# Optimization experiments

Hardware: AMD Instinct MI355X
Metric: run time of the kernel (lower is better)

Reference implementation:

```python
import jax, jax.numpy as jnp
import numpy as np

NUM_HEADS = 16


def setup_inputs() -> dict:
    key = jax.random.key(0)
    ks = jax.random.split(key, 5)
    N, L, E = 4, 1024, 1024
    x = jax.random.normal(ks[0], (N, L, E), dtype=jnp.float32)
    sc = 1.0 / np.sqrt(E)
    wq = jax.random.normal(ks[1], (E, E), dtype=jnp.float32) * sc
    wk = jax.random.normal(ks[2], (E, E), dtype=jnp.float32) * sc
    wv = jax.random.normal(ks[3], (E, E), dtype=jnp.float32) * sc
    wo = jax.random.normal(ks[4], (E, E), dtype=jnp.float32) * sc
    return {"x": x, "wq": wq, "wk": wk, "wv": wv, "wo": wo}


def reference(x, wq, wk, wv, wo):
    N, L, E = x.shape
    H = NUM_HEADS
    d = E // H  # d_k = d_v = d_q
    # Linear layers: y = x @ W^T (torch Linear weight is (out, in))
    q = (x @ wq.T).reshape(N, H, L, d)  # NOTE: raw view, matches torch .view
    k = (x @ wk.T).reshape(N, H, L, d)
    v = (x @ wv.T).reshape(N, H, L, d)
    scores = jnp.einsum("nhld,nhmd->nhlm", q, k) / jnp.sqrt(jnp.float32(d))
    # causal mask (dropout is identity in eval / p=0)
    causal = jnp.tril(jnp.ones((L, L), dtype=bool))
    scores = jnp.where(causal, scores, jnp.float32(-jnp.inf))
    attn = jax.nn.softmax(scores, axis=-1)
    wei = jnp.einsum("nhlm,nhmd->nhld", attn, v).reshape(N, L, H * d)
    return wei @ wo.T
```

## Files before the change

### kernel.cpp

```cpp
#include <hip/hip_runtime.h>
#include <hip/hip_bf16.h>

using bf16 = __hip_bfloat16;
typedef __attribute__((ext_vector_type(8))) short bf16x8;
typedef __attribute__((ext_vector_type(4))) float f32x4;

#define MFMA16(a, b, c) __builtin_amdgcn_mfma_f32_16x16x32_bf16(a, b, c, 0, 0, 0)
#define SWZ(row, byteoff) ((byteoff) ^ (((row) & 7) << 4))

__device__ __forceinline__ unsigned short f2b(float f) {
  union { float f; unsigned int u; } c; c.f = f;
  unsigned int r = c.u + 0x7fffu + ((c.u >> 16) & 1u);
  return (unsigned short)(r >> 16);
}
__device__ __forceinline__ float b2f(short b) {
  union { unsigned int u; float f; } c;
  c.u = ((unsigned int)(unsigned short)b) << 16;
  return c.f;
}
__device__ __forceinline__ bf16x8 scale8(bf16x8 v, float s) {
  bf16x8 r;
#pragma unroll
  for (int j = 0; j < 8; ++j) r[j] = (short)f2b(b2f(v[j]) * s);
  return r;
}
__device__ __forceinline__ unsigned cvtpk(float a, float b) {
  unsigned r;
  asm("v_cvt_pk_bf16_f32 %0, %1, %2" : "=v"(r) : "v"(a), "v"(b));
  return r;
}

__device__ __forceinline__ void gload_lds16(const void* g, void* l) {
  __builtin_amdgcn_global_load_lds(
      (const __attribute__((address_space(1))) void*)g,
      (__attribute__((address_space(3))) void*)l, 16, 0, 0);
}

__device__ __forceinline__ void store_out(float* p, float v) { *p = v; }
__device__ __forceinline__ void store_out(bf16* p, float v) {
  *(unsigned short*)p = f2b(v);
}

__global__ __launch_bounds__(256) void cast_all(
    const float* __restrict__ x, const float* __restrict__ wq,
    const float* __restrict__ wk, const float* __restrict__ wv,
    const float* __restrict__ wo,
    unsigned short* __restrict__ xb, unsigned short* __restrict__ wqb,
    unsigned short* __restrict__ wkb, unsigned short* __restrict__ wvb,
    unsigned short* __restrict__ wob) {
  int i = blockIdx.x * 256 + threadIdx.x;
  const float* src;
  unsigned short* dst;
  int off;
  if (i < 1048576) {
    src = x; dst = xb; off = i;
  } else {
    int j = i - 1048576;
    int seg = j >> 18;
    off = j & 262143;
    src = (seg == 0) ? wq : (seg == 1) ? wk : (seg == 2) ? wv : wo;
    dst = (seg == 0) ? wqb : (seg == 1) ? wkb : (seg == 2) ? wvb : wob;
  }
  float4 v = reinterpret_cast<const float4*>(src)[off];
  ushort4 o;
  o.x = f2b(v.x); o.y = f2b(v.y); o.z = f2b(v.z); o.w = f2b(v.w);
  reinterpret_cast<ushort4*>(dst)[off] = o;
}

template <typename TOUT>
__device__ __forceinline__ void gemm_tile(const bf16* __restrict__ A,
                                          const bf16* __restrict__ Bt,
                                          TOUT* __restrict__ C, int N, int K,
                                          int bm, int bn) {
  __shared__ bf16 Asm[128 * 64];
  __shared__ bf16 Bsm[128 * 64];
  const int tid = threadIdx.x;
  const int lane = tid & 63;
  const int w = tid >> 6;
  const int wr = w >> 1, wc = w & 1;
  const int fr = lane & 15;
  const int fg = lane >> 4;
  f32x4 acc[4][4] = {};

  const int strow = w * 8 + (lane >> 3);
  const int stcb = (lane & 7) * 16;

  for (int kt = 0; kt < K; kt += 64) {
#pragma unroll
    for (int r = 0; r < 4; ++r) {
      const int row = r * 32 + strow;
      gload_lds16(
          (const char*)(A + (size_t)(bm + row) * K + kt) + SWZ(row, stcb),
          (char*)Asm + (r * 32 + w * 8) * 128);
      gload_lds16(
          (const char*)(Bt + (size_t)row * K + kt) + SWZ(row, stcb),
          (char*)Bsm + (r * 32 + w * 8) * 128);
    }
    __syncthreads();
    bf16x8 afr[4][2], bfr[4][2];
#pragma unroll
    for (int m = 0; m < 4; ++m) {
      const int row = wr * 64 + m * 16 + fr;
      const char* rp = (const char*)Asm + row * 128;
#pragma unroll
      for (int s = 0; s < 2; ++s)
        afr[m][s] = *(const bf16x8*)(rp + SWZ(row, s * 64 + fg * 16));
    }
#pragma unroll
    for (int n = 0; n < 4; ++n) {
      const int row = wc * 64 + n * 16 + fr;
      const char* rp = (const char*)Bsm + row * 128;
#pragma unroll
      for (int s = 0; s < 2; ++s)
        bfr[n][s] = *(const bf16x8*)(rp + SWZ(row, s * 64 + fg * 16));
    }
    __builtin_amdgcn_s_setprio(1);
#pragma unroll
    for (int m = 0; m < 4; ++m)
#pragma unroll
      for (int n = 0; n < 4; ++n) {
        acc[m][n] = MFMA16(afr[m][0], bfr[n][0], acc[m][n]);
        acc[m][n] = MFMA16(afr[m][1], bfr[n][1], acc[m][n]);
      }
    __builtin_amdgcn_s_setprio(0);
    __syncthreads();
  }
#pragma unroll
  for (int m = 0; m < 4; ++m) {
    const int row0 = bm + wr * 64 + m * 16 + (lane >> 4) * 4;
#pragma unroll
    for (int n = 0; n < 4; ++n) {
      const int col = bn + wc * 64 + n * 16 + fr;
#pragma unroll
      for (int r = 0; r < 4; ++r)
        store_out(&C[(size_t)(row0 + r) * N + col], acc[m][n][r]);
    }
  }
}

__global__ __launch_bounds__(256) void gemm_qkv(
    const bf16* __restrict__ A, const bf16* __restrict__ B3,
    bf16* __restrict__ Cq, bf16* __restrict__ Ck, bf16* __restrict__ Cv) {
  const int id = blockIdx.y * 32 + blockIdx.x;
  const int sw = (id & 7) * 96 + (id >> 3);
  const int bm = (sw & 31) * 128;
  const int bnG = (sw >> 5) * 128;
  bf16* C = (bnG < 1024) ? Cq : (bnG < 2048) ? Ck : Cv;
  gemm_tile<bf16>(A, B3 + (size_t)bnG * 1024, C, 1024, 1024, bm, bnG & 1023);
}

__global__ __launch_bounds__(256) void gemm_out64(const bf16* __restrict__ A,
                                                  const bf16* __restrict__ B,
                                                  float* __restrict__ C) {
  __shared__ bf16 Asm[128 * 64];
  __shared__ bf16 Bsm[64 * 64];
  const int id = blockIdx.y * 32 + blockIdx.x;
  const int sw = (id & 7) * 64 + (id >> 3);
  const int bm = (sw & 31) * 128;
  const int bn = (sw >> 5) * 64;
  const bf16* Bt = B + (size_t)bn * 1024;

  const int tid = threadIdx.x;
  const int lane = tid & 63;
  const int w = tid >> 6;
  const int wr = w >> 1, wc = w & 1;
  const int fr = lane & 15;
  const int fg = lane >> 4;
  f32x4 acc[4][2] = {};

  const int strow = w * 8 + (lane >> 3);
  const int stcb = (lane & 7) * 16;

  for (int kt = 0; kt < 1024; kt += 64) {
#pragma unroll
    for (int r = 0; r < 4; ++r) {
      const int row = r * 32 + strow;
      gload_lds16(
          (const char*)(A + (size_t)(bm + row) * 1024 + kt) + SWZ(row, stcb),
          (char*)Asm + (r * 32 + w * 8) * 128);
    }
#pragma unroll
    for (int r = 0; r < 2; ++r) {
      const int row = r * 32 + strow;
      gload_lds16(
          (const char*)(Bt + (size_t)row * 1024 + kt) + SWZ(row, stcb),
          (char*)Bsm + (r * 32 + w * 8) * 128);
    }
    __syncthreads();
    bf16x8 afr[4][2], bfr[2][2];
#pragma unroll
    for (int m = 0; m < 4; ++m) {
      const int row = wr * 64 + m * 16 + fr;
      const char* rp = (const char*)Asm + row * 128;
#pragma unroll
      for (int s = 0; s < 2; ++s)
        afr[m][s] = *(const bf16x8*)(rp + SWZ(row, s * 64 + fg * 16));
    }
#pragma unroll
    for (int n = 0; n < 2; ++n) {
      const int row = wc * 32 + n * 16 + fr;
      const char* rp = (const char*)Bsm + row * 128;
#pragma unroll
      for (int s = 0; s < 2; ++s)
        bfr[n][s] = *(const bf16x8*)(rp + SWZ(row, s * 64 + fg * 16));
    }
    __builtin_amdgcn_s_setprio(1);
#pragma unroll
    for (int m = 0; m < 4; ++m)
#pragma unroll
      for (int n = 0; n < 2; ++n) {
        acc[m][n] = MFMA16(afr[m][0], bfr[n][0], acc[m][n]);
        acc[m][n] = MFMA16(afr[m][1], bfr[n][1], acc[m][n]);
      }
    __builtin_amdgcn_s_setprio(0);
    __syncthreads();
  }
#pragma unroll
  for (int m = 0; m < 4; ++m) {
    const int row0 = bm + wr * 64 + m * 16 + fg * 4;
#pragma unroll
    for (int n = 0; n < 2; ++n) {
      const int col = bn + wc * 32 + n * 16 + fr;
#pragma unroll
      for (int r = 0; r < 4; ++r)
        C[(size_t)(row0 + r) * 1024 + col] = acc[m][n][r];
    }
  }
}

__global__ __launch_bounds__(256) void attn_fwd(
    const bf16* __restrict__ Q, const bf16* __restrict__ K,
    const bf16* __restrict__ V, bf16* __restrict__ O) {
  const int nh = blockIdx.x;
  const size_t base = (size_t)nh * 65536;
  const bf16* Qp = Q + base;
  const bf16* Kp = K + base;
  const bf16* Vp = V + base;
  bf16* Op = O + base;
  const int p = blockIdx.y;
  const int qiA = p, qiB = 15 - p;
  const int tid = threadIdx.x;
  const int lane = tid & 63;
  const int w = tid >> 6;
  const int fr = lane & 15;
  const int fg = lane >> 4;

  __shared__ bf16 Ksm[2][2][64 * 64];
  __shared__ bf16 Vts[2][2][64 * 64];

  const float QSC = 0.125f * 1.44269504089f;
  const float MS = 12.0f;
  const int rA0 = qiA * 64 + w * 16;
  const int rB0 = qiB * 64 + w * 16;
  bf16x8 qA[2], qB[2];
#pragma unroll
  for (int ks = 0; ks < 2; ++ks) {
    qA[ks] = scale8(
        *(const bf16x8*)&Qp[(size_t)(rA0 + fr) * 64 + ks * 32 + fg * 8], QSC);
    qB[ks] = scale8(
        *(const bf16x8*)&Qp[(size_t)(rB0 + fr) * 64 + ks * 32 + fg * 8], QSC);
  }

  float sA = 0.f, sB = 0.f;
  f32x4 oA[4], oB[4];
#pragma unroll
  for (int d = 0; d < 4; ++d) {
    oA[d] = (f32x4){0.f, 0.f, 0.f, 0.f};
    oB[d] = (f32x4){0.f, 0.f, 0.f, 0.f};
  }

  const int NKV = qiB + 1;
  const int qloc = w * 16 + fr;

  const int bkv = (tid & 15) * 4;
  const int bd = (tid >> 4) * 4;
  union VU { ushort4 v; unsigned short s[4]; };
  VU v4a[4], v4b[4];

  const int krow = w * 16 + (lane >> 3);
  const int kcb = (lane & 7) * 16;

#define STAGE_K(kt, dst)                                                      \
  {                                                                           \
    _Pragma("unroll") for (int i = 0; i < 2; ++i) {                           \
      const int row = krow + i * 8;                                           \
      gload_lds16((const char*)Kp + ((size_t)((kt)*64 + row) * 128 +          \
                                     SWZ(row, kcb)),                          \
                  (char*)(dst) + (w * 16 + i * 8) * 128);                     \
    }                                                                         \
  }
#define LOAD_V(kt, r)                                                         \
  {                                                                           \
    _Pragma("unroll") for (int j = 0; j < 4; ++j) (r)[j].v =                  \
        *(const ushort4*)(Vp + (size_t)((kt)*64 + bkv + j) * 64 + bd);        \
  }
#define WRITE_V(dst, r)                                                       \
  {                                                                           \
    _Pragma("unroll") for (int i = 0; i < 4; ++i) {                           \
      VU o4;                                                                  \
      _Pragma("unroll") for (int j = 0; j < 4; ++j) o4.s[j] = (r)[j].s[i];    \
      const int row = bd + i;                                                 \
      *(ushort4*)((char*)(dst) + row * 128 + SWZ(row, bkv * 2)) = o4.v;       \
    }                                                                         \
  }

  union PU { bf16x8 v; unsigned u[4]; };
  union VF { bf16x8 v; unsigned long long q[2]; };

  auto compute_tile = [&](int kt, const char* kb, const char* vb) {
    const bool aAct = (kt <= qiA);
    bf16x8 kf[4][2];
#pragma unroll
    for (int c = 0; c < 4; ++c) {
      const int row = c * 16 + fr;
      const char* rp = kb + row * 128;
      kf[c][0] = *(const bf16x8*)(rp + SWZ(row, fg * 16));
      kf[c][1] = *(const bf16x8*)(rp + SWZ(row, 64 + fg * 16));
    }
    VF vf[4][2];
#pragma unroll
    for (int d = 0; d < 4; ++d) {
      const int row = d * 16 + fr;
      const char* rp = vb + row * 128;
#pragma unroll
      for (int ks = 0; ks < 2; ++ks) {
        vf[d][ks].q[0] =
            *(const unsigned long long*)(rp + SWZ(row, ks * 64 + fg * 8));
        vf[d][ks].q[1] =
            *(const unsigned long long*)(rp + SWZ(row, ks * 64 + 32 + fg * 8));
      }
    }

    auto strip_sm = [&](const bf16x8 (&qf)[2], float& s, bool diag,
                        PU (&pa)[2]) {
      f32x4 sc[4];
      __builtin_amdgcn_s_setprio(1);
#pragma unroll
      for (int c = 0; c < 4; ++c) {
        f32x4 acc = (f32x4){0.f, 0.f, 0.f, 0.f};
        acc = MFMA16(kf[c][0], qf[0], acc);
        acc = MFMA16(kf[c][1], qf[1], acc);
        sc[c] = acc;
      }
      __builtin_amdgcn_s_setprio(0);
      float pv[4][4];
#pragma unroll
      for (int c = 0; c < 4; ++c)
#pragma unroll
        for (int r = 0; r < 4; ++r) {
          float sv = sc[c][r];
          if (diag) {
            const int kvloc = c * 16 + fg * 4 + r;
            sv = (kvloc <= qloc) ? sv : -INFINITY;
          }
          const float e = __builtin_amdgcn_exp2f(sv - MS);
          pv[c][r] = e;
          s += e;
        }
#pragma unroll
      for (int ks = 0; ks < 2; ++ks) {
        pa[ks].u[0] = cvtpk(pv[ks * 2][0], pv[ks * 2][1]);
        pa[ks].u[1] = cvtpk(pv[ks * 2][2], pv[ks * 2][3]);
        pa[ks].u[2] = cvtpk(pv[ks * 2 + 1][0], pv[ks * 2 + 1][1]);
        pa[ks].u[3] = cvtpk(pv[ks * 2 + 1][2], pv[ks * 2 + 1][3]);
      }
    };

    PU paA[2], paB[2];
    strip_sm(qB, sB, kt == qiB, paB);
    if (aAct) strip_sm(qA, sA, kt == qiA, paA);

    __builtin_amdgcn_s_setprio(1);
#pragma unroll
    for (int d = 0; d < 4; ++d) {
      oB[d] = MFMA16(paB[0].v, vf[d][0].v, oB[d]);
      oB[d] = MFMA16(paB[1].v, vf[d][1].v, oB[d]);
    }
    if (aAct) {
#pragma unroll
      for (int d = 0; d < 4; ++d) {
        oA[d] = MFMA16(paA[0].v, vf[d][0].v, oA[d]);
        oA[d] = MFMA16(paA[1].v, vf[d][1].v, oA[d]);
      }
    }
    __builtin_amdgcn_s_setprio(0);
  };

  STAGE_K(0, &Ksm[0][0][0]);
  STAGE_K(1, &Ksm[0][1][0]);
  LOAD_V(0, v4a);
  LOAD_V(1, v4b);
  WRITE_V(&Vts[0][0][0], v4a);
  WRITE_V(&Vts[0][1][0], v4b);
  __syncthreads();

  const int I = (NKV + 1) >> 1;
  for (int it = 0; it < I; ++it) {
    const int kt0 = 2 * it;
    const int b = it & 1;
    const bool more0 = (kt0 + 2 < NKV);
    const bool more1 = (kt0 + 3 < NKV);
    if (more0) {
      STAGE_K(kt0 + 2, &Ksm[b ^ 1][0][0]);
      LOAD_V(kt0 + 2, v4a);
    }
    if (more1) {
      STAGE_K(kt0 + 3, &Ksm[b ^ 1][1][0]);
      LOAD_V(kt0 + 3, v4b);
    }

    compute_tile(kt0, (const char*)&Ksm[b][0][0], (const char*)&Vts[b][0][0]);
    if (kt0 + 1 < NKV)
      compute_tile(kt0 + 1, (const char*)&Ksm[b][1][0],
                   (const char*)&Vts[b][1][0]);

    if (more0) WRITE_V(&Vts[b ^ 1][0][0], v4a);
    if (more1) WRITE_V(&Vts[b ^ 1][1][0], v4b);
    __syncthreads();
  }

  sA += __shfl_xor(sA, 16); sA += __shfl_xor(sA, 32);
  sB += __shfl_xor(sB, 16); sB += __shfl_xor(sB, 32);
  float sAo[4], sBo[4];
#pragma unroll
  for (int r = 0; r < 4; ++r) {
    sAo[r] = __shfl(sA, fg * 4 + r);
    sBo[r] = __shfl(sB, fg * 4 + r);
  }

#pragma unroll
  for (int d = 0; d < 4; ++d)
#pragma unroll
    for (int r = 0; r < 4; ++r) {
      const float vA = oA[d][r] / sAo[r];
      const float vB = oB[d][r] / sBo[r];
      *(unsigned short*)&Op[(size_t)(rA0 + fg * 4 + r) * 64 + d * 16 + fr] =
          f2b(vA);
      *(unsigned short*)&Op[(size_t)(rB0 + fg * 4 + r) * 64 + d * 16 + fr] =
          f2b(vB);
    }
#undef STAGE_K
#undef LOAD_V
#undef WRITE_V
}

extern "C" void kernel_launch(void* const* d_in, const int* in_sizes, int n_in,
                              void* d_out, int out_size, void* d_ws,
                              size_t ws_size, hipStream_t stream) {
  const float* x = (const float*)d_in[0];
  const float* wq = (const float*)d_in[1];
  const float* wk = (const float*)d_in[2];
  const float* wv = (const float*)d_in[3];
  const float* wo = (const float*)d_in[4];
  float* out = (float*)d_out;
  char* ws = (char*)d_ws;

  bf16* xb = (bf16*)(ws);
  bf16* wqkv = (bf16*)(ws + (8u << 20));
  bf16* wqb = wqkv;
  bf16* wkb = (bf16*)(ws + (10u << 20));
  bf16* wvb = (bf16*)(ws + (12u << 20));
  bf16* wob = (bf16*)(ws + (14u << 20));
  bf16* qbuf = (bf16*)(ws + (16u << 20));
  bf16* kbuf = (bf16*)(ws + (24u << 20));
  bf16* vbuf = (bf16*)(ws + (32u << 20));
  bf16* weib = (bf16*)(ws);

  cast_all<<<8192, 256, 0, stream>>>(x, wq, wk, wv, wo, (unsigned short*)xb,
                                     (unsigned short*)wqb, (unsigned short*)wkb,
                                     (unsigned short*)wvb, (unsigned short*)wob);
  gemm_qkv<<<dim3(32, 24), 256, 0, stream>>>(xb, wqkv, qbuf, kbuf, vbuf);
  attn_fwd<<<dim3(64, 8), 256, 0, stream>>>(qbuf, kbuf, vbuf, weib);
  gemm_out64<<<dim3(32, 16), 256, 0, stream>>>(weib, wob, out);
}
```

Before: 86.74 us.

## Rewrite QKV GEMM as 256x256 8-wave kernel with 4-stage LDS pipeline

Replaces the 128x128 single-buffered QKV projection GEMM with a 512-thread, 256x256-tile kernel. It streams 32-wide K slices through a four-slot LDS ring using global_load_lds, with explicit vmcnt/lgkmcnt waits and barriers so loads overlap MFMA work. The larger tile raises arithmetic intensity per block and removes per-iteration full syncs. The cost is a grid of only 192 blocks, which may underfill the GPU, plus fragile hand-scheduled wait counts and much higher register use.

New measurement: 95.17 us. +9.7%, slower.

```diff
diff --git a/kernel.cpp b/kernel.cpp
--- a/kernel.cpp
+++ b/kernel.cpp
@@ -7,6 +7,7 @@
 
 #define MFMA16(a, b, c) __builtin_amdgcn_mfma_f32_16x16x32_bf16(a, b, c, 0, 0, 0)
 #define SWZ(row, byteoff) ((byteoff) ^ (((row) & 7) << 4))
+#define SWZ64(row, byteoff) ((byteoff) ^ ((((row) >> 1) & 3) << 4))
 
 __device__ __forceinline__ unsigned short f2b(float f) {
   union { float f; unsigned int u; } c; c.f = f;
@@ -34,11 +35,6 @@
   __builtin_amdgcn_global_load_lds(
       (const __attribute__((address_space(1))) void*)g,
       (__attribute__((address_space(3))) void*)l, 16, 0, 0);
-}
-
-__device__ __forceinline__ void store_out(float* p, float v) { *p = v; }
-__device__ __forceinline__ void store_out(bf16* p, float v) {
-  *(unsigned short*)p = f2b(v);
 }
 
 __global__ __launch_bounds__(256) void cast_all(
@@ -67,86 +63,161 @@
   reinterpret_cast<ushort4*>(dst)[off] = o;
 }
 
-template <typename TOUT>
-__device__ __forceinline__ void gemm_tile(const bf16* __restrict__ A,
-                                          const bf16* __restrict__ Bt,
-                                          TOUT* __restrict__ C, int N, int K,
-                                          int bm, int bn) {
-  __shared__ bf16 Asm[128 * 64];
-  __shared__ bf16 Bsm[128 * 64];
+__global__ __launch_bounds__(512, 2) void gemm_qkv8(
+    const bf16* __restrict__ A, const bf16* __restrict__ B3,
+    bf16* __restrict__ Cq, bf16* __restrict__ Ck, bf16* __restrict__ Cv) {
+  __shared__ bf16 As[4][256 * 32];
+  __shared__ bf16 Bs[4][256 * 32];
   const int tid = threadIdx.x;
   const int lane = tid & 63;
   const int w = tid >> 6;
-  const int wr = w >> 1, wc = w & 1;
+  const int wr = w >> 2;
+  const int wc = w & 3;
   const int fr = lane & 15;
   const int fg = lane >> 4;
-  f32x4 acc[4][4] = {};
-
-  const int strow = w * 8 + (lane >> 3);
-  const int stcb = (lane & 7) * 16;
-
-  for (int kt = 0; kt < K; kt += 64) {
-#pragma unroll
-    for (int r = 0; r < 4; ++r) {
-      const int row = r * 32 + strow;
-      gload_lds16(
-          (const char*)(A + (size_t)(bm + row) * K + kt) + SWZ(row, stcb),
-          (char*)Asm + (r * 32 + w * 8) * 128);
-      gload_lds16(
-          (const char*)(Bt + (size_t)row * K + kt) + SWZ(row, stcb),
-          (char*)Bsm + (r * 32 + w * 8) * 128);
-    }
-    __syncthreads();
-    bf16x8 afr[4][2], bfr[4][2];
-#pragma unroll
-    for (int m = 0; m < 4; ++m) {
-      const int row = wr * 64 + m * 16 + fr;
-      const char* rp = (const char*)Asm + row * 128;
-#pragma unroll
-      for (int s = 0; s < 2; ++s)
-        afr[m][s] = *(const bf16x8*)(rp + SWZ(row, s * 64 + fg * 16));
-    }
-#pragma unroll
-    for (int n = 0; n < 4; ++n) {
-      const int row = wc * 64 + n * 16 + fr;
-      const char* rp = (const char*)Bsm + row * 128;
-#pragma unroll
-      for (int s = 0; s < 2; ++s)
-        bfr[n][s] = *(const bf16x8*)(rp + SWZ(row, s * 64 + fg * 16));
-    }
+
+  const int id = blockIdx.y * 16 + blockIdx.x;
+  const int sw = (id & 7) * 24 + (id >> 3);
+  const int bm = (sw & 15) * 256;
+  const int bnG = (sw >> 4) * 256;
+  const bf16* Bt = B3 + (size_t)bnG * 1024;
+  bf16* C = (bnG < 1024) ? Cq : (bnG < 2048) ? Ck : Cv;
+  const int bn = bnG & 1023;
+
+  const int srow = tid >> 2;
+  const int scb = (tid & 3) * 16;
+
+  f32x4 acc[8][4] = {};
+
+#define QST(P, RB, t, kh, s, ARR)                                            \
+  {                                                                          \
+    _Pragma("unroll") for (int rr = 0; rr < 2; ++rr) {                       \
+      const int row = rr * 128 + srow;                                       \
+      gload_lds16((const char*)(P) +                                         \
+                      ((size_t)((RB) + row) * 1024 + (t)*64 + (kh)*32) * 2 + \
+                      SWZ64(row, scb),                                       \
+                  (char*)&ARR[s][0] + rr * 8192 + tid * 16);                 \
+    }                                                                        \
+  }
+#define AFR(s, m)                                                           \
+  (*(const bf16x8*)((const char*)&As[s][0] +                                \
+                    (wr * 128 + (m)*16 + fr) * 64 +                         \
+                    SWZ64(wr * 128 + (m)*16 + fr, fg * 16)))
+#define BFR(s, n)                                                           \
+  (*(const bf16x8*)((const char*)&Bs[s][0] +                                \
+                    (wc * 64 + (n)*16 + fr) * 64 +                          \
+                    SWZ64(wc * 64 + (n)*16 + fr, fg * 16)))
+#define LGKM0                                             \
+  asm volatile("s_waitcnt lgkmcnt(0)" ::: "memory");      \
+  __builtin_amdgcn_sched_barrier(0)
+
+  QST(A, bm, 0, 0, 0, As);
+  QST(Bt, 0, 0, 0, 0, Bs);
+  QST(A, bm, 0, 1, 1, As);
+  QST(Bt, 0, 0, 1, 1, Bs);
+  QST(A, bm, 1, 0, 2, As);
+  QST(Bt, 0, 1, 0, 2, Bs);
+  asm volatile("s_waitcnt vmcnt(8)" ::: "memory");
+  __builtin_amdgcn_sched_barrier(0);
+  __builtin_amdgcn_s_barrier();
+
+  for (int t = 0; t < 16; ++t) {
+    const int s0 = (2 * t) & 3, s1 = (2 * t + 1) & 3;
+    const int sn1 = (2 * t + 3) & 3;
+    const int sn2 = (2 * t + 4) & 3;
+    bf16x8 af[8], b0, b1;
+
+#pragma unroll
+    for (int m = 0; m < 8; ++m) af[m] = AFR(s0, m);
+    b0 = BFR(s0, 0);
+    b1 = BFR(s0, 1);
+    if (t < 15) QST(A, bm, t + 1, 1, sn1, As);
+    __builtin_amdgcn_s_barrier();
+    LGKM0;
     __builtin_amdgcn_s_setprio(1);
 #pragma unroll
-    for (int m = 0; m < 4; ++m)
-#pragma unroll
-      for (int n = 0; n < 4; ++n) {
-        acc[m][n] = MFMA16(afr[m][0], bfr[n][0], acc[m][n]);
-        acc[m][n] = MFMA16(afr[m][1], bfr[n][1], acc[m][n]);
-      }
+    for (int m = 0; m < 8; ++m) {
+      acc[m][0] = MFMA16(af[m], b0, acc[m][0]);
+      acc[m][1] = MFMA16(af[m], b1, acc[m][1]);
+    }
     __builtin_amdgcn_s_setprio(0);
-    __syncthreads();
-  }
-#pragma unroll
-  for (int m = 0; m < 4; ++m) {
-    const int row0 = bm + wr * 64 + m * 16 + (lane >> 4) * 4;
+    __builtin_amdgcn_s_barrier();
+
+    b0 = BFR(s0, 2);
+    b1 = BFR(s0, 3);
+    if (t < 15) QST(Bt, 0, t + 1, 1, sn1, Bs);
+    __builtin_amdgcn_s_barrier();
+    LGKM0;
+    __builtin_amdgcn_s_setprio(1);
+#pragma unroll
+    for (int m = 0; m < 8; ++m) {
+      acc[m][2] = MFMA16(af[m], b0, acc[m][2]);
+      acc[m][3] = MFMA16(af[m], b1, acc[m][3]);
+    }
+    __builtin_amdgcn_s_setprio(0);
+    if (t < 15) {
+      asm volatile("s_waitcnt vmcnt(8)" ::: "memory");
+    } else {
+      asm volatile("s_waitcnt vmcnt(0)" ::: "memory");
+    }
+    __builtin_amdgcn_sched_barrier(0);
+    __builtin_amdgcn_s_barrier();
+
+#pragma unroll
+    for (int m = 0; m < 8; ++m) af[m] = AFR(s1, m);
+    b0 = BFR(s1, 0);
+    b1 = BFR(s1, 1);
+    if (t < 14) QST(A, bm, t + 2, 0, sn2, As);
+    __builtin_amdgcn_s_barrier();
+    LGKM0;
+    __builtin_amdgcn_s_setprio(1);
+#pragma unroll
+    for (int m = 0; m < 8; ++m) {
+      acc[m][0] = MFMA16(af[m], b0, acc[m][0]);
+      acc[m][1] = MFMA16(af[m], b1, acc[m][1]);
+    }
+    __builtin_amdgcn_s_setprio(0);
+    __builtin_amdgcn_s_barrier();
+
+    b0 = BFR(s1, 2);
+    b1 = BFR(s1, 3);
+    if (t < 14) QST(Bt, 0, t + 2, 0, sn2, Bs);
+    __builtin_amdgcn_s_barrier();
+    LGKM0;
+    __builtin_amdgcn_s_setprio(1);
+#pragma unroll
+    for (int m = 0; m < 8; ++m) {
+      acc[m][2] = MFMA16(af[m], b0, acc[m][2]);
+      acc[m][3] = MFMA16(af[m], b1, acc[m][3]);
+    }
+    __builtin_amdgcn_s_setprio(0);
+    if (t <= 13) {
+      asm volatile("s_waitcnt vmcnt(8)" ::: "memory");
+      __builtin_amdgcn_sched_barrier(0);
+      __builtin_amdgcn_s_barrier();
+    } else if (t == 14) {
+      asm volatile("s_waitcnt vmcnt(4)" ::: "memory");
+      __builtin_amdgcn_sched_barrier(0);
+      __builtin_amdgcn_s_barrier();
+    }
+  }
+
+#pragma unroll
+  for (int m = 0; m < 8; ++m) {
+    const int row0 = bm + wr * 128 + m * 16 + fg * 4;
 #pragma unroll
     for (int n = 0; n < 4; ++n) {
       const int col = bn + wc * 64 + n * 16 + fr;
 #pragma unroll
       for (int r = 0; r < 4; ++r)
-        store_out(&C[(size_t)(row0 + r) * N + col], acc[m][n][r]);
-    }
-  }
-}
-
-__global__ __launch_bounds__(256) void gemm_qkv(
-    const bf16* __restrict__ A, const bf16* __restrict__ B3,
-    bf16* __restrict__ Cq, bf16* __restrict__ Ck, bf16* __restrict__ Cv) {
-  const int id = blockIdx.y * 32 + blockIdx.x;
-  const int sw = (id & 7) * 96 + (id >> 3);
-  const int bm = (sw & 31) * 128;
-  const int bnG = (sw >> 5) * 128;
-  bf16* C = (bnG < 1024) ? Cq : (bnG < 2048) ? Ck : Cv;
-  gemm_tile<bf16>(A, B3 + (size_t)bnG * 1024, C, 1024, 1024, bm, bnG & 1023);
+        *(unsigned short*)&C[(size_t)(row0 + r) * 1024 + col] =
+            f2b(acc[m][n][r]);
+    }
+  }
+#undef QST
+#undef AFR
+#undef BFR
+#undef LGKM0
 }
 
 __global__ __launch_bounds__(256) void gemm_out64(const bf16* __restrict__ A,
@@ -469,7 +540,7 @@
   cast_all<<<8192, 256, 0, stream>>>(x, wq, wk, wv, wo, (unsigned short*)xb,
                                      (unsigned short*)wqb, (unsigned short*)wkb,
                                      (unsigned short*)wvb, (unsigned short*)wob);
-  gemm_qkv<<<dim3(32, 24), 256, 0, stream>>>(xb, wqkv, qbuf, kbuf, vbuf);
+  gemm_qkv8<<<dim3(16, 12), 512, 0, stream>>>(xb, wqkv, qbuf, kbuf, vbuf);
   attn_fwd<<<dim3(64, 8), 256, 0, stream>>>(qbuf, kbuf, vbuf, weib);
   gemm_out64<<<dim3(32, 16), 256, 0, stream>>>(weib, wob, out);
 }
```
